# Kernel tuning notes

Hardware: AMD Instinct MI355X
Metric: run time of the kernel (lower is better)

## Reference

```python
import jax, jax.numpy as jnp
import numpy as np

DIM, HEADS, WS = 256, 16, 8
B, H, W = 2, 252, 252
BN_EPS = 1e-5


def _rel_index():
    # Same construction as the torch buffer relative_position_index (64,64)
    coords = np.stack(np.meshgrid(np.arange(WS), np.arange(WS), indexing='ij'))
    flat = coords.reshape(2, -1)
    rel = (flat[:, :, None] - flat[:, None, :]).transpose(1, 2, 0).copy()
    rel[..., 0] += WS - 1
    rel[..., 1] += WS - 1
    rel[..., 0] *= 2 * WS - 1
    return jnp.asarray(rel.sum(-1))

REL_IDX = _rel_index()  # (WS*WS, WS*WS) int


def _conv(x, w, pad, groups=1):
    return jax.lax.conv_general_dilated(
        x, w, (1, 1), [(pad[0], pad[0]), (pad[1], pad[1])],
        dimension_numbers=('NCHW', 'OIHW', 'NCHW'), feature_group_count=groups)


def setup_inputs() -> dict:
    key = jax.random.key(0)
    ks = jax.random.split(key, 8)
    s = lambda k, shape, sc: jax.random.normal(k, shape, jnp.float32) * sc
    z = lambda: jnp.zeros((DIM,), jnp.float32)
    return {
        'x': s(ks[0], (B, DIM, H, W), 1.0),
        'w_qkv': s(ks[1], (3 * DIM, DIM, 1, 1), 0.05),
        'rel_bias_table': s(ks[2], ((2 * WS - 1) ** 2, HEADS), 0.02),
        'w_h': s(ks[3], (DIM, DIM, WS, 1), 0.02),
        'b_h': z(),
        'w_v': s(ks[4], (DIM, DIM, 1, WS), 0.02),
        'b_v': z(),
        'w_dw': s(ks[5], (DIM, 1, WS, WS), 0.05),
        'bn_gamma': jnp.ones((DIM,), jnp.float32),
        'bn_beta': z(),
        'bn_mean': z(),
        'bn_var': jnp.ones((DIM,), jnp.float32),
        'w_pw': s(ks[6], (DIM, DIM, 1, 1), 0.05),
    }


def reference(x, w_qkv, rel_bias_table, w_h, b_h, w_v, b_v, w_dw,
              bn_gamma, bn_beta, bn_mean, bn_var, w_pw):
    Bc, C, Hc, Wc = x.shape
    pad_h, pad_w = WS - Hc % WS, WS - Wc % WS
    xp = jnp.pad(x, ((0, 0), (0, 0), (0, pad_h), (0, pad_w)), mode='reflect')
    Hp, Wp = Hc + pad_h, Wc + pad_w
    hh, ww, d = Hp // WS, Wp // WS, C // HEADS

    qkv = _conv(xp, w_qkv, (0, 0))  # (B, 3C, Hp, Wp)
    # b (qkv h d) (hh ws1) (ww ws2) -> qkv (b hh ww) h (ws1 ws2) d
    qkv = qkv.reshape(Bc, 3, HEADS, d, hh, WS, ww, WS)
    qkv = qkv.transpose(1, 0, 4, 6, 2, 5, 7, 3).reshape(3, Bc * hh * ww, HEADS, WS * WS, d)
    q, k, v = qkv[0], qkv[1], qkv[2]

    dots = jnp.einsum('nhid,nhjd->nhij', q, k) * (d ** -0.5)
    bias = rel_bias_table[REL_IDX.reshape(-1)].reshape(WS * WS, WS * WS, HEADS)
    dots = dots + bias.transpose(2, 0, 1)[None]  # (1, h, 64, 64)
    attn = jax.nn.softmax(dots, axis=-1)
    out = jnp.einsum('nhij,nhjd->nhid', attn, v)
    # (b hh ww) h (ws1 ws2) d -> b (h d) (hh ws1) (ww ws2)
    out = out.reshape(Bc, hh, ww, HEADS, WS, WS, d)
    out = out.transpose(0, 3, 6, 1, 4, 2, 5).reshape(Bc, C, Hp, Wp)
    out = out[:, :, :Hc, :Wc]

    p1 = _conv(jnp.pad(out, ((0, 0), (0, 0), (0, 1), (0, 0)), mode='reflect'),
               w_h, (WS // 2 - 1, 0)) + b_h[None, :, None, None]
    p2 = _conv(jnp.pad(out, ((0, 0), (0, 0), (0, 0), (0, 1)), mode='reflect'),
               w_v, (0, WS // 2 - 1)) + b_v[None, :, None, None]
    y = jnp.pad(p1 + p2, ((0, 0), (0, 0), (0, 1), (0, 1)), mode='reflect')
    y = _conv(y, w_dw, ((WS - 1) // 2, (WS - 1) // 2), groups=DIM)  # depthwise
    inv = bn_gamma / jnp.sqrt(bn_var + BN_EPS)
    y = y * inv[None, :, None, None] + (bn_beta - bn_mean * inv)[None, :, None, None]
    y = _conv(y, w_pw, (0, 0))  # pointwise 1x1
    return y[:, :, :Hc, :Wc]
```

## Files before the change

kernel.cpp:

```cpp
#include <hip/hip_runtime.h>
#include <hip/hip_bf16.h>

#define HC 252
#define WC 252
#define CD 256
#define NHEADS 16

#define XP_W 264
#define XP_HW (252*264)
#define XP_CHW (256*252*264)

typedef unsigned short u16;
typedef unsigned int u32;
typedef __attribute__((ext_vector_type(8))) short bf16x8;
typedef __attribute__((ext_vector_type(4))) float f32x4;
typedef __attribute__((ext_vector_type(4))) u32 u32x4;
typedef __attribute__((ext_vector_type(2))) u32 u32x2;

#define XP_BYTES (2u * (unsigned)XP_CHW * 2u)
#define ZP_OFF   XP_BYTES
#define ZP_BYTES 409600u
#define WT_OFF   (ZP_OFF + ZP_BYTES)
#define WT_ELEMS (128*8192)
#define WPW_OFF  (WT_OFF + (unsigned)WT_ELEMS*2u)
#define WPW_ELEMS (8*8192)
#define WQ_OFF   (WPW_OFF + (unsigned)WPW_ELEMS*2u)
#define WQ_ELEMS (768*256)
#define BIAS_OFF (WQ_OFF + (unsigned)WQ_ELEMS*2u)

__device__ __forceinline__ u16 bfu(float f) {
    __hip_bfloat16 h = __float2bfloat16(f);
    return *(reinterpret_cast<u16*>(&h));
}
__device__ __forceinline__ u32 pack2(float a, float b) {
    return (u32)bfu(a) | ((u32)bfu(b) << 16);
}

__global__ __launch_bounds__(256, 2) void attn_mfma(
    const float* __restrict__ x, const u16* __restrict__ WQ,
    const float* __restrict__ BIASF, u16* __restrict__ xp)
{
    __shared__ __align__(16) char smem[73728];

    const int bid = blockIdx.x;
    const int zz = (bid & 7) * 256 + (bid >> 3);
    const int wx = zz & 31, wy = (zz >> 5) & 31, b = zz >> 10;
    const int tid = threadIdx.x;
    const int lane = tid & 63, wid = tid >> 6;
    const int g = lane >> 4, li = lane & 15;

    {
        int ci = tid;
        const float* srcc = x + (size_t)(b * 256 + ci) * (HC * WC);
        #pragma unroll
        for (int r = 0; r < 8; ++r) {
            int h = wy * 8 + r; if (h >= HC) h = 2 * HC - 2 - h;
            const float* src = srcc + h * WC;
            float v[8];
            if (wx == 31) {
                #pragma unroll
                for (int c = 0; c < 8; ++c) {
                    int w = 248 + c; if (w >= WC) w = 2 * WC - 2 - w;
                    v[c] = src[w];
                }
            } else {
                float4 f0 = *(const float4*)(src + wx * 8);
                float4 f1 = *(const float4*)(src + wx * 8 + 4);
                v[0]=f0.x; v[1]=f0.y; v[2]=f0.z; v[3]=f0.w;
                v[4]=f1.x; v[5]=f1.y; v[6]=f1.z; v[7]=f1.w;
            }
            #pragma unroll
            for (int c = 0; c < 8; ++c) {
                int pos = r * 8 + c;
                int byte = pos * 512 + ((ci * 2) ^ ((pos & 7) << 4));
                *(u16*)(smem + byte) = bfu(v[c]);
            }
        }
    }
    __syncthreads();

    const int WB = 32768 + wid * 10240;
    char* Qb = smem + WB;
    char* Kb = smem + WB + 2048;
    char* Vb = smem + WB + 4096;
    char* Pb = smem + WB + 6144;

    const bf16x8 zf = {0,0,0,0,0,0,0,0};

    #pragma unroll 1
    for (int hh = 0; hh < 4; ++hh) {
        const int head = wid * 4 + hh;

        f32x4 acc[3][4];
        #pragma unroll
        for (int p = 0; p < 3; ++p)
            #pragma unroll
            for (int nf = 0; nf < 4; ++nf) acc[p][nf] = (f32x4){0.f,0.f,0.f,0.f};

        for (int ks = 0; ks < 8; ++ks) {
            bf16x8 bx[4];
            #pragma unroll
            for (int nf = 0; nf < 4; ++nf) {
                int pos = 16 * nf + li;
                int byte = pos * 512 + ((ks * 64 + 16 * g) ^ ((pos & 7) << 4));
                bx[nf] = *(const bf16x8*)(smem + byte);
            }
            bf16x8 aw[3];
            #pragma unroll
            for (int p = 0; p < 3; ++p) {
                int o = p * 256 + head * 16 + li;
                aw[p] = *(const bf16x8*)(WQ + o * 256 + ks * 32 + 8 * g);
            }
            __builtin_amdgcn_s_setprio(1);
            #pragma unroll
            for (int p = 0; p < 3; ++p)
                #pragma unroll
                for (int nf = 0; nf < 4; ++nf)
                    acc[p][nf] = __builtin_amdgcn_mfma_f32_16x16x32_bf16(aw[p], bx[nf], acc[p][nf], 0, 0, 0);
            __builtin_amdgcn_s_setprio(0);
        }

        #pragma unroll
        for (int p = 0; p < 3; ++p) {
            if (p < 2) {
                char* base = (p == 0) ? Qb : Kb;
                #pragma unroll
                for (int nf = 0; nf < 4; ++nf) {
                    int pos = 16 * nf + li;
                    u32 lo = pack2(acc[p][nf][0], acc[p][nf][1]);
                    u32 hi = pack2(acc[p][nf][2], acc[p][nf][3]);
                    int byte = pos * 32 + ((8 * g) ^ (((pos >> 2) & 1) << 4));
                    *(u32x2*)(base + byte) = (u32x2){lo, hi};
                }
            } else {
                #pragma unroll
                for (int nf = 0; nf < 4; ++nf) {
                    int pos = 16 * nf + li;
                    #pragma unroll
                    for (int r = 0; r < 4; ++r) {
                        int d = 4 * g + r;
                        int byte = (pos >> 3) * 256 + d * 16 + (pos & 7) * 2;
                        *(u16*)(Vb + byte) = bfu(acc[p][nf][r]);
                    }
                }
            }
        }

        f32x4 s[4][4];
        #pragma unroll
        for (int mf = 0; mf < 4; ++mf)
            #pragma unroll
            for (int nf = 0; nf < 4; ++nf) s[mf][nf] = (f32x4){0.f,0.f,0.f,0.f};
        bf16x8 bk[4];
        #pragma unroll
        for (int nf = 0; nf < 4; ++nf) {
            int pos = 16 * nf + li;
            bk[nf] = (g < 2) ? *(const bf16x8*)(Kb + pos * 32 + ((16 * g) ^ (((pos >> 2) & 1) << 4))) : zf;
        }
        __builtin_amdgcn_s_setprio(1);
        #pragma unroll
        for (int mf = 0; mf < 4; ++mf) {
            int pos = 16 * mf + li;
            bf16x8 aq = (g < 2) ? *(const bf16x8*)(Qb + pos * 32 + ((16 * g) ^ (((pos >> 2) & 1) << 4))) : zf;
            #pragma unroll
            for (int nf = 0; nf < 4; ++nf)
                s[mf][nf] = __builtin_amdgcn_mfma_f32_16x16x32_bf16(aq, bk[nf], s[mf][nf], 0, 0, 0);
        }
        __builtin_amdgcn_s_setprio(0);

        f32x4 e[4][4];
        f32x4 rs[4];
        #pragma unroll
        for (int mf = 0; mf < 4; ++mf) rs[mf] = (f32x4){0.f,0.f,0.f,0.f};
        #pragma unroll
        for (int mf = 0; mf < 4; ++mf)
            #pragma unroll
            for (int nf = 0; nf < 4; ++nf) {
                f32x4 b4 = *(const f32x4*)(BIASF + (((head * 4 + mf) * 4 + nf) * 64 + lane) * 4);
                #pragma unroll
                for (int r = 0; r < 4; ++r) {
                    float ev = __expf(s[mf][nf][r] * 0.25f + b4[r]);
                    e[mf][nf][r] = ev;
                    rs[mf][r] += ev;
                }
            }
        #pragma unroll
        for (int mf = 0; mf < 4; ++mf)
            #pragma unroll
            for (int r = 0; r < 4; ++r) {
                float t = rs[mf][r];
                t += __shfl_xor(t, 1); t += __shfl_xor(t, 2);
                t += __shfl_xor(t, 4); t += __shfl_xor(t, 8);
                rs[mf][r] = t;
            }

        f32x4 o[4];
        #pragma unroll
        for (int mf = 0; mf < 4; ++mf) o[mf] = (f32x4){0.f,0.f,0.f,0.f};
        const bool even = !(lane & 1);
        #pragma unroll
        for (int hf = 0; hf < 2; ++hf) {
            #pragma unroll
            for (int mf = 0; mf < 4; ++mf)
                #pragma unroll
                for (int nfl = 0; nfl < 2; ++nfl) {
                    f32x4 ee = e[mf][2 * hf + nfl];
                    float p0 = __shfl_xor(ee[0], 1), p1 = __shfl_xor(ee[1], 1);
                    float p2 = __shfl_xor(ee[2], 1), p3 = __shfl_xor(ee[3], 1);
                    int jl = 16 * nfl + (li & ~1);
                    u32 w0, w1; int r0;
                    if (even) { w0 = pack2(ee[0], p0); w1 = pack2(ee[1], p1); r0 = 0; }
                    else      { w0 = pack2(p2, ee[2]); w1 = pack2(p3, ee[3]); r0 = 2; }
                    int i0 = 16 * mf + 4 * g + r0, i1 = i0 + 1;
                    *(u32*)(Pb + i0 * 64 + ((2 * jl) ^ ((i0 & 3) << 4))) = w0;
                    *(u32*)(Pb + i1 * 64 + ((2 * jl) ^ ((i1 & 3) << 4))) = w1;
                }
            bf16x8 bv = *(const bf16x8*)(Vb + (4 * hf + g) * 256 + li * 16);
            __builtin_amdgcn_s_setprio(1);
            #pragma unroll
            for (int mf = 0; mf < 4; ++mf) {
                int i = 16 * mf + li;
                bf16x8 ap = *(const bf16x8*)(Pb + i * 64 + ((16 * g) ^ ((i & 3) << 4)));
                o[mf] = __builtin_amdgcn_mfma_f32_16x16x32_bf16(ap, bv, o[mf], 0, 0, 0);
            }
            __builtin_amdgcn_s_setprio(0);
        }

        #pragma unroll
        for (int mf = 0; mf < 4; ++mf) {
            int h = wy * 8 + 2 * mf + (g >> 1);
            int wbase = wx * 8 + 4 * (g & 1);
            if (h < HC && wbase < WC) {
                float v0 = o[mf][0] / rs[mf][0], v1 = o[mf][1] / rs[mf][1];
                float v2 = o[mf][2] / rs[mf][2], v3 = o[mf][3] / rs[mf][3];
                size_t idx = ((size_t)(b * 256 + head * 16 + li) * HC + h) * XP_W + wbase + 4;
                *(u32x2*)(xp + idx) = (u32x2){pack2(v0, v1), pack2(v2, v3)};
            }
        }
    }
}

__global__ __launch_bounds__(256) void wprep_kernel(
    const float* __restrict__ wh, const float* __restrict__ wv,
    const float* __restrict__ wpw, const float* __restrict__ wqkv,
    const float* __restrict__ btab, u16* __restrict__ wsu)
{
    int i = blockIdx.x * 256 + threadIdx.x;
    u16* WT = wsu + WT_OFF / 2;
    u16* WP = wsu + WPW_OFF / 2;
    u16* ZP = wsu + ZP_OFF / 2;
    u16* WQp = wsu + WQ_OFF / 2;
    float* BF = (float*)(wsu + BIAS_OFF / 2);
    if (i < WT_ELEMS) {
        int j = i & 7, co = (i >> 3) & 255, kb = (i >> 11) & 3, s = i >> 13;
        float v = (s < 64) ? wh[co * 2048 + s * 32 + kb * 8 + j]
                           : wv[co * 2048 + (s - 64) * 32 + kb * 8 + j];
        WT[i] = bfu(v);
    } else if (i < WT_ELEMS + WPW_ELEMS) {
        int i2 = i - WT_ELEMS;
        int j = i2 & 7, co = (i2 >> 3) & 255, kb = (i2 >> 11) & 3, s = i2 >> 13;
        WP[i2] = bfu(wpw[co * 256 + s * 32 + kb * 8 + j]);
    } else if (i < WT_ELEMS + WPW_ELEMS + (int)(ZP_BYTES / 2)) {
        ZP[i - WT_ELEMS - WPW_ELEMS] = 0;
    } else if (i < WT_ELEMS + WPW_ELEMS + (int)(ZP_BYTES / 2) + WQ_ELEMS) {
        int i4 = i - WT_ELEMS - WPW_ELEMS - (int)(ZP_BYTES / 2);
        WQp[i4] = bfu(wqkv[i4]);
    } else {
        int i5 = i - WT_ELEMS - WPW_ELEMS - (int)(ZP_BYTES / 2) - WQ_ELEMS;
        if (i5 < 16384) {
            int lane = i5 & 63, nf = (i5 >> 6) & 3, mf = (i5 >> 8) & 3, head = i5 >> 10;
            int gg = lane >> 4, ll = lane & 15;
            #pragma unroll
            for (int r = 0; r < 4; ++r) {
                int row = 16 * mf + 4 * gg + r;
                int col = 16 * nf + ll;
                int dy = (row >> 3) - (col >> 3) + 7;
                int dx = (row & 7) - (col & 7) + 7;
                BF[i5 * 4 + r] = btab[(dy * 15 + dx) * NHEADS + head];
            }
        }
    }
}

__global__ __launch_bounds__(256) void halo_kernel(u16* __restrict__ xp)
{
    int i = blockIdx.x * 256 + threadIdx.x;
    if (i >= 129024 * 12) return;
    int row = i / 12, c = i % 12;
    int wp = (c < 4) ? c : 252 + c;
    u16 v = 0;
    if (wp == 256) v = xp[row * XP_W + 254];
    xp[row * XP_W + wp] = v;
}

__global__ __launch_bounds__(512, 2) void sepconv_mfma(
    const u16* __restrict__ xp, const u16* __restrict__ WT,
    const u16* __restrict__ ZP,
    const float* __restrict__ b_h, const float* __restrict__ b_v,
    float* __restrict__ P)
{
    __shared__ u16 As[2][8192];
    __shared__ u16 Bs[2][256 * 36];

    const int bid = blockIdx.x;
    const int zz = (bid & 7) * 63 + (bid >> 3);
    const int h = zz % HC, b = zz / HC;
    const int tid = threadIdx.x;
    const int lane = tid & 63, wid = tid >> 6;
    const int wr = wid >> 2, wc = wid & 3;
    const int cq = lane & 15, kb = lane >> 4;

    const int wl2 = (tid & 127) * 2;
    const int oc = tid >> 7;

    const u16* hcur[8];
    int hstep[8];
    #pragma unroll
    for (int t = 0; t < 8; ++t) {
        int j = h + t - 3;
        bool valid = (j >= 0 && j <= 252);
        int jr = (j == 252) ? 250 : j;
        hcur[t] = valid ? (xp + (size_t)b * XP_CHW + (size_t)jr * XP_W) : ZP;
        hstep[t] = valid ? 4 * XP_HW : 0;
    }
    const u16* vbase = xp + (size_t)b * XP_CHW + (size_t)h * XP_W;
    const int hvoff = oc * XP_HW + wl2 + 4;

    const int bw0 = wl2 * 36 + oc * 8;
    const int bw1 = bw0 + 36;

    f32x4 acc[8][4];
    #pragma unroll
    for (int m = 0; m < 8; ++m)
        #pragma unroll
        for (int n = 0; n < 4; ++n) acc[m][n] = (f32x4){0.f, 0.f, 0.f, 0.f};

    u32x4 rA[2];
    u32 rB[8];

    int aw0, aw1;
    {
        int c0 = tid, c1 = 512 + tid;
        aw0 = ((c0 >> 8) * 256 + ((c0 & 255) ^ (((c0 >> 8) & 3) << 1))) * 8;
        aw1 = ((c1 >> 8) * 256 + ((c1 & 255) ^ (((c1 >> 8) & 3) << 1))) * 8;
    }

    rA[0] = *(const u32x4*)(WT + (size_t)tid * 8);
    rA[1] = *(const u32x4*)(WT + (size_t)(512 + tid) * 8);
    #pragma unroll
    for (int t = 0; t < 8; ++t)
        rB[t] = *(const u32*)(hcur[t] + hvoff);
    *(u32x4*)&As[0][aw0] = rA[0];
    *(u32x4*)&As[0][aw1] = rA[1];
    {
        union { bf16x8 v; u32 u[4]; } p0, p1;
        #pragma unroll
        for (int q = 0; q < 4; ++q) {
            p0.u[q] = __builtin_amdgcn_perm(rB[2 * q + 1], rB[2 * q], 0x05040100u);
            p1.u[q] = __builtin_amdgcn_perm(rB[2 * q + 1], rB[2 * q], 0x07060302u);
        }
        *(bf16x8*)&Bs[0][bw0] = p0.v;
        *(bf16x8*)&Bs[0][bw1] = p1.v;
    }

    for (int s = 0; s < 128; ++s) {
        const int cur = s & 1;
        const int s1 = s + 1;
        const bool hph1 = (s1 < 64);
        if (s1 < 128) {
            rA[0] = *(const u32x4*)(WT + (size_t)s1 * 8192 + (size_t)tid * 8);
            rA[1] = *(const u32x4*)(WT + (size_t)s1 * 8192 + (size_t)(512 + tid) * 8);
            if (hph1) {
                #pragma unroll
                for (int t = 0; t < 8; ++t) hcur[t] += hstep[t];
                #pragma unroll
                for (int t = 0; t < 8; ++t)
                    rB[t] = *(const u32*)(hcur[t] + hvoff);
            } else {
                int off = ((s1 - 64) * 4 + oc) * XP_HW + wl2;
                #pragma unroll
                for (int l = 0; l < 6; ++l)
                    rB[l] = *(const u32*)(vbase + off + 2 * l);
            }
        }
        __syncthreads();

        bf16x8 af[8], bfr[4];
        #pragma unroll
        for (int m = 0; m < 8; ++m) {
            int row = wr * 128 + m * 16 + cq;
            af[m] = *(const bf16x8*)&As[cur][(kb * 256 + (row ^ (kb << 1))) * 8];
        }
        #pragma unroll
        for (int n = 0; n < 4; ++n)
            bfr[n] = *(const bf16x8*)&Bs[cur][(wc * 64 + n * 16 + cq) * 36 + kb * 8];
        #pragma unroll
        for (int m = 0; m < 8; ++m)
            #pragma unroll
            for (int n = 0; n < 4; ++n)
                acc[m][n] = __builtin_amdgcn_mfma_f32_16x16x32_bf16(af[m], bfr[n], acc[m][n], 0, 0, 0);

        if (s1 < 128) {
            const int nxt = cur ^ 1;
            *(u32x4*)&As[nxt][aw0] = rA[0];
            *(u32x4*)&As[nxt][aw1] = rA[1];
            union { bf16x8 v; u32 u[4]; } p0, p1;
            if (hph1) {
                #pragma unroll
                for (int q = 0; q < 4; ++q) {
                    p0.u[q] = __builtin_amdgcn_perm(rB[2 * q + 1], rB[2 * q], 0x05040100u);
                    p1.u[q] = __builtin_amdgcn_perm(rB[2 * q + 1], rB[2 * q], 0x07060302u);
                }
            } else {
                #pragma unroll
                for (int q = 0; q < 4; ++q)
                    p0.u[q] = __builtin_amdgcn_alignbit(rB[q + 1], rB[q], 16);
                p1.u[0] = rB[1]; p1.u[1] = rB[2];
                p1.u[2] = rB[3]; p1.u[3] = rB[4];
            }
            *(bf16x8*)&Bs[nxt][bw0] = p0.v;
            *(bf16x8*)&Bs[nxt][bw1] = p1.v;
        }
    }

    const int rq = lane >> 4, cc = lane & 15;
    #pragma unroll
    for (int m = 0; m < 8; ++m) {
        int cgb = wr * 128 + m * 16 + rq * 4;
        float bias[4];
        #pragma unroll
        for (int rr = 0; rr < 4; ++rr) bias[rr] = b_h[cgb + rr] + b_v[cgb + rr];
        #pragma unroll
        for (int n = 0; n < 4; ++n) {
            int wg = wc * 64 + n * 16 + cc;
            if (wg < WC) {
                #pragma unroll
                for (int rr = 0; rr < 4; ++rr)
                    P[((size_t)(b * CD + cgb + rr) * HC + h) * WC + wg] = acc[m][n][rr] + bias[rr];
            }
        }
    }
}

__global__ __launch_bounds__(256) void dwbn_kernel(
    const float* __restrict__ P, const float* __restrict__ w_dw,
    const float* __restrict__ gamma, const float* __restrict__ beta,
    const float* __restrict__ mean, const float* __restrict__ var,
    __hip_bfloat16* __restrict__ Yb)
{
    __shared__ float ps[15][42];
    __shared__ float wd[64];
    const int bw = blockIdx.x, bh = blockIdx.y, bz = blockIdx.z;
    const int b = bz >> 8, c = bz & 255;
    const int h0 = bh * 8, w0 = bw * 32;
    const int tid = threadIdx.x;
    if (tid < 64) wd[tid] = w_dw[c * 64 + tid];
    for (int it = 0; it < 3; ++it) {
        int flat = tid + it * 256;
        if (flat < 630) {
            int row = flat / 42, col = flat % 42;
            int j = h0 - 3 + row, wcol = w0 - 3 + col;
            float v = 0.f;
            if (j >= 0 && j <= HC && wcol >= 0 && wcol <= WC) {
                int jr = (j == HC) ? (HC - 2) : j;
                int wr2 = (wcol == WC) ? (WC - 2) : wcol;
                v = P[((b * CD + c) * HC + jr) * WC + wr2];
            }
            ps[row][col] = v;
        }
    }
    __syncthreads();
    const int r = tid >> 5, cc = tid & 31;
    const int h = h0 + r, w = w0 + cc;
    if (h < HC && w < WC) {
        float s = 0.f;
        #pragma unroll
        for (int u = 0; u < 8; ++u)
            #pragma unroll
            for (int v2 = 0; v2 < 8; ++v2)
                s += wd[u * 8 + v2] * ps[r + u][cc + v2];
        const float inv = gamma[c] * rsqrtf(var[c] + 1e-5f);
        Yb[((b * CD + c) * HC + h) * WC + w] = __float2bfloat16(s * inv + (beta[c] - mean[c] * inv));
    }
}

__global__ __launch_bounds__(512, 2) void pw_mfma(
    const u16* __restrict__ Y, const u16* __restrict__ WP,
    float* __restrict__ O)
{
    __shared__ u16 As[2][8192];
    __shared__ u16 Bs[2][256 * 36];

    const int bid = blockIdx.x;
    const int zz = (bid & 7) * 63 + (bid >> 3);
    const int h = zz % HC, b = zz / HC;
    const int tid = threadIdx.x;
    const int lane = tid & 63, wid = tid >> 6;
    const int wr = wid >> 2, wc = wid & 3;
    const int cq = lane & 15, kb = lane >> 4;

    const int wl2 = (tid & 127) * 2;
    const int oc = tid >> 7;

    const u16* yb = Y + ((size_t)(b * 256 + oc * 8) * HC + h) * WC + wl2;

    const int bw0 = wl2 * 36 + oc * 8;
    const int bw1 = bw0 + 36;

    f32x4 acc[8][4];
    #pragma unroll
    for (int m = 0; m < 8; ++m)
        #pragma unroll
        for (int n = 0; n < 4; ++n) acc[m][n] = (f32x4){0.f, 0.f, 0.f, 0.f};

    u32x4 rA[2];
    u32 rB[8];

    int aw0, aw1;
    {
        int c0 = tid, c1 = 512 + tid;
        aw0 = ((c0 >> 8) * 256 + ((c0 & 255) ^ (((c0 >> 8) & 3) << 1))) * 8;
        aw1 = ((c1 >> 8) * 256 + ((c1 & 255) ^ (((c1 >> 8) & 3) << 1))) * 8;
    }

    rA[0] = *(const u32x4*)(WP + (size_t)tid * 8);
    rA[1] = *(const u32x4*)(WP + (size_t)(512 + tid) * 8);
    #pragma unroll
    for (int j = 0; j < 8; ++j)
        rB[j] = *(const u32*)(yb + (size_t)j * (HC * WC));
    *(u32x4*)&As[0][aw0] = rA[0];
    *(u32x4*)&As[0][aw1] = rA[1];
    {
        union { bf16x8 v; u32 u[4]; } p0, p1;
        #pragma unroll
        for (int q = 0; q < 4; ++q) {
            p0.u[q] = __builtin_amdgcn_perm(rB[2 * q + 1], rB[2 * q], 0x05040100u);
            p1.u[q] = __builtin_amdgcn_perm(rB[2 * q + 1], rB[2 * q], 0x07060302u);
        }
        *(bf16x8*)&Bs[0][bw0] = p0.v;
        *(bf16x8*)&Bs[0][bw1] = p1.v;
    }

    for (int s = 0; s < 8; ++s) {
        const int cur = s & 1;
        const int s1 = s + 1;
        if (s1 < 8) {
            rA[0] = *(const u32x4*)(WP + (size_t)s1 * 8192 + (size_t)tid * 8);
            rA[1] = *(const u32x4*)(WP + (size_t)s1 * 8192 + (size_t)(512 + tid) * 8);
            #pragma unroll
            for (int j = 0; j < 8; ++j)
                rB[j] = *(const u32*)(yb + (size_t)(s1 * 32 + j) * (HC * WC));
        }
        __syncthreads();

        bf16x8 af[8], bfr[4];
        #pragma unroll
        for (int m = 0; m < 8; ++m) {
            int row = wr * 128 + m * 16 + cq;
            af[m] = *(const bf16x8*)&As[cur][(kb * 256 + (row ^ (kb << 1))) * 8];
        }
        #pragma unroll
        for (int n = 0; n < 4; ++n)
            bfr[n] = *(const bf16x8*)&Bs[cur][(wc * 64 + n * 16 + cq) * 36 + kb * 8];
        #pragma unroll
        for (int m = 0; m < 8; ++m)
            #pragma unroll
            for (int n = 0; n < 4; ++n)
                acc[m][n] = __builtin_amdgcn_mfma_f32_16x16x32_bf16(af[m], bfr[n], acc[m][n], 0, 0, 0);

        if (s1 < 8) {
            const int nxt = cur ^ 1;
            *(u32x4*)&As[nxt][aw0] = rA[0];
            *(u32x4*)&As[nxt][aw1] = rA[1];
            union { bf16x8 v; u32 u[4]; } p0, p1;
            #pragma unroll
            for (int q = 0; q < 4; ++q) {
                p0.u[q] = __builtin_amdgcn_perm(rB[2 * q + 1], rB[2 * q], 0x05040100u);
                p1.u[q] = __builtin_amdgcn_perm(rB[2 * q + 1], rB[2 * q], 0x07060302u);
            }
            *(bf16x8*)&Bs[nxt][bw0] = p0.v;
            *(bf16x8*)&Bs[nxt][bw1] = p1.v;
        }
    }

    const int rq = lane >> 4, cc = lane & 15;
    #pragma unroll
    for (int m = 0; m < 8; ++m) {
        int cgb = wr * 128 + m * 16 + rq * 4;
        #pragma unroll
        for (int n = 0; n < 4; ++n) {
            int wg = wc * 64 + n * 16 + cc;
            if (wg < WC) {
                #pragma unroll
                for (int rr = 0; rr < 4; ++rr)
                    O[((size_t)(b * CD + cgb + rr) * HC + h) * WC + wg] = acc[m][n][rr];
            }
        }
    }
}

extern "C" void kernel_launch(void* const* d_in, const int* in_sizes, int n_in,
                              void* d_out, int out_size, void* d_ws, size_t ws_size,
                              hipStream_t stream)
{
    const float* x      = (const float*)d_in[0];
    const float* w_qkv  = (const float*)d_in[1];
    const float* bias_t = (const float*)d_in[2];
    const float* w_h    = (const float*)d_in[3];
    const float* b_h    = (const float*)d_in[4];
    const float* w_v    = (const float*)d_in[5];
    const float* b_v    = (const float*)d_in[6];
    const float* w_dw   = (const float*)d_in[7];
    const float* bn_g   = (const float*)d_in[8];
    const float* bn_b   = (const float*)d_in[9];
    const float* bn_m   = (const float*)d_in[10];
    const float* bn_v   = (const float*)d_in[11];
    const float* w_pw   = (const float*)d_in[12];
    float* out = (float*)d_out;

    u16* wsu = (u16*)d_ws;
    const u16* XPu = wsu;
    const u16* ZPu = wsu + ZP_OFF / 2;
    const u16* WTu = wsu + WT_OFF / 2;
    const u16* WPu = wsu + WPW_OFF / 2;
    const u16* WQu = wsu + WQ_OFF / 2;
    const float* BFu = (const float*)(wsu + BIAS_OFF / 2);

    wprep_kernel<<<5984, 256, 0, stream>>>(w_h, w_v, w_pw, w_qkv, bias_t, wsu);
    attn_mfma<<<2048, 256, 0, stream>>>(x, WQu, BFu, wsu);
    halo_kernel<<<6048, 256, 0, stream>>>(wsu);
    sepconv_mfma<<<504, 512, 0, stream>>>(XPu, WTu, ZPu, b_h, b_v, out);
    dwbn_kernel<<<dim3(8, 32, 512), 256, 0, stream>>>(out, w_dw, bn_g, bn_b, bn_m, bn_v,
                                                      (__hip_bfloat16*)d_ws);
    pw_mfma<<<504, 512, 0, stream>>>(wsu, WPu, out);
}
```

Measured before the change: 677.1 us.

## Store sepconv output as bf16, pre-swizzle weights, raise MFMA priority

The separable-conv intermediate P is now written as bf16 instead of fp32 and converted back in the depthwise/BN kernel, halving that round-trip's memory traffic at a small precision cost. Weight tiles for sepconv and pointwise GEMMs are pre-swizzled in the prep kernel, so the LDS stores use a linear address and the per-thread swizzle math goes away. The MFMA blocks are wrapped in s_setprio raises, and the main loops are marked unroll 1 to limit code size and register pressure.

```diff
diff --git a/kernel.cpp b/kernel.cpp
--- a/kernel.cpp
+++ b/kernel.cpp
@@ -34,6 +34,9 @@
 }
 __device__ __forceinline__ u32 pack2(float a, float b) {
     return (u32)bfu(a) | ((u32)bfu(b) << 16);
+}
+__device__ __forceinline__ float bf2f(u16 v) {
+    union { u32 u; float f; } cv; cv.u = ((u32)v) << 16; return cv.f;
 }
 
 __global__ __launch_bounds__(256, 2) void attn_mfma(
@@ -252,13 +255,17 @@
     u16* WQp = wsu + WQ_OFF / 2;
     float* BF = (float*)(wsu + BIAS_OFF / 2);
     if (i < WT_ELEMS) {
-        int j = i & 7, co = (i >> 3) & 255, kb = (i >> 11) & 3, s = i >> 13;
+        int j = i & 7, l = (i >> 3) & 1023, s = i >> 13;
+        int kb = (l >> 8) & 3;
+        int co = (l & 255) ^ (kb << 1);
         float v = (s < 64) ? wh[co * 2048 + s * 32 + kb * 8 + j]
                            : wv[co * 2048 + (s - 64) * 32 + kb * 8 + j];
         WT[i] = bfu(v);
     } else if (i < WT_ELEMS + WPW_ELEMS) {
         int i2 = i - WT_ELEMS;
-        int j = i2 & 7, co = (i2 >> 3) & 255, kb = (i2 >> 11) & 3, s = i2 >> 13;
+        int j = i2 & 7, l = (i2 >> 3) & 1023, s = i2 >> 13;
+        int kb = (l >> 8) & 3;
+        int co = (l & 255) ^ (kb << 1);
         WP[i2] = bfu(wpw[co * 256 + s * 32 + kb * 8 + j]);
     } else if (i < WT_ELEMS + WPW_ELEMS + (int)(ZP_BYTES / 2)) {
         ZP[i - WT_ELEMS - WPW_ELEMS] = 0;
@@ -297,10 +304,10 @@
     const u16* __restrict__ xp, const u16* __restrict__ WT,
     const u16* __restrict__ ZP,
     const float* __restrict__ b_h, const float* __restrict__ b_v,
-    float* __restrict__ P)
+    u16* __restrict__ P)
 {
-    __shared__ u16 As[2][8192];
-    __shared__ u16 Bs[2][256 * 36];
+    __shared__ __align__(16) u16 As[2][8192];
+    __shared__ __align__(16) u16 Bs[2][256 * 36];
 
     const int bid = blockIdx.x;
     const int zz = (bid & 7) * 63 + (bid >> 3);
@@ -338,20 +345,13 @@
     u32x4 rA[2];
     u32 rB[8];
 
-    int aw0, aw1;
-    {
-        int c0 = tid, c1 = 512 + tid;
-        aw0 = ((c0 >> 8) * 256 + ((c0 & 255) ^ (((c0 >> 8) & 3) << 1))) * 8;
-        aw1 = ((c1 >> 8) * 256 + ((c1 & 255) ^ (((c1 >> 8) & 3) << 1))) * 8;
-    }
-
     rA[0] = *(const u32x4*)(WT + (size_t)tid * 8);
     rA[1] = *(const u32x4*)(WT + (size_t)(512 + tid) * 8);
     #pragma unroll
     for (int t = 0; t < 8; ++t)
         rB[t] = *(const u32*)(hcur[t] + hvoff);
-    *(u32x4*)&As[0][aw0] = rA[0];
-    *(u32x4*)&As[0][aw1] = rA[1];
+    *(u32x4*)&As[0][(size_t)tid * 8] = rA[0];
+    *(u32x4*)&As[0][(size_t)(512 + tid) * 8] = rA[1];
     {
         union { bf16x8 v; u32 u[4]; } p0, p1;
         #pragma unroll
@@ -363,6 +363,7 @@
         *(bf16x8*)&Bs[0][bw1] = p1.v;
     }
 
+    #pragma unroll 1
     for (int s = 0; s < 128; ++s) {
         const int cur = s & 1;
         const int s1 = s + 1;
@@ -385,25 +386,29 @@
         }
         __syncthreads();
 
-        bf16x8 af[8], bfr[4];
-        #pragma unroll
-        for (int m = 0; m < 8; ++m) {
-            int row = wr * 128 + m * 16 + cq;
-            af[m] = *(const bf16x8*)&As[cur][(kb * 256 + (row ^ (kb << 1))) * 8];
-        }
-        #pragma unroll
-        for (int n = 0; n < 4; ++n)
-            bfr[n] = *(const bf16x8*)&Bs[cur][(wc * 64 + n * 16 + cq) * 36 + kb * 8];
-        #pragma unroll
-        for (int m = 0; m < 8; ++m)
+        {
+            bf16x8 af[8], bfr[4];
+            #pragma unroll
+            for (int m = 0; m < 8; ++m) {
+                int row = wr * 128 + m * 16 + cq;
+                af[m] = *(const bf16x8*)&As[cur][(kb * 256 + (row ^ (kb << 1))) * 8];
+            }
             #pragma unroll
             for (int n = 0; n < 4; ++n)
-                acc[m][n] = __builtin_amdgcn_mfma_f32_16x16x32_bf16(af[m], bfr[n], acc[m][n], 0, 0, 0);
+                bfr[n] = *(const bf16x8*)&Bs[cur][(wc * 64 + n * 16 + cq) * 36 + kb * 8];
+            __builtin_amdgcn_s_setprio(1);
+            #pragma unroll
+            for (int m = 0; m < 8; ++m)
+                #pragma unroll
+                for (int n = 0; n < 4; ++n)
+                    acc[m][n] = __builtin_amdgcn_mfma_f32_16x16x32_bf16(af[m], bfr[n], acc[m][n], 0, 0, 0);
+            __builtin_amdgcn_s_setprio(0);
+        }
 
         if (s1 < 128) {
             const int nxt = cur ^ 1;
-            *(u32x4*)&As[nxt][aw0] = rA[0];
-            *(u32x4*)&As[nxt][aw1] = rA[1];
+            *(u32x4*)&As[nxt][(size_t)tid * 8] = rA[0];
+            *(u32x4*)&As[nxt][(size_t)(512 + tid) * 8] = rA[1];
             union { bf16x8 v; u32 u[4]; } p0, p1;
             if (hph1) {
                 #pragma unroll
@@ -436,14 +441,14 @@
             if (wg < WC) {
                 #pragma unroll
                 for (int rr = 0; rr < 4; ++rr)
-                    P[((size_t)(b * CD + cgb + rr) * HC + h) * WC + wg] = acc[m][n][rr] + bias[rr];
+                    P[((size_t)(b * CD + cgb + rr) * HC + h) * WC + wg] = bfu(acc[m][n][rr] + bias[rr]);
             }
         }
     }
 }
 
 __global__ __launch_bounds__(256) void dwbn_kernel(
-    const float* __restrict__ P, const float* __restrict__ w_dw,
+    const u16* __restrict__ P, const float* __restrict__ w_dw,
     const float* __restrict__ gamma, const float* __restrict__ beta,
     const float* __restrict__ mean, const float* __restrict__ var,
     __hip_bfloat16* __restrict__ Yb)
@@ -464,7 +469,7 @@
             if (j >= 0 && j <= HC && wcol >= 0 && wcol <= WC) {
                 int jr = (j == HC) ? (HC - 2) : j;
                 int wr2 = (wcol == WC) ? (WC - 2) : wcol;
-                v = P[((b * CD + c) * HC + jr) * WC + wr2];
+                v = bf2f(P[((size_t)(b * CD + c) * HC + jr) * WC + wr2]);
             }
             ps[row][col] = v;
         }
@@ -488,8 +493,8 @@
     const u16* __restrict__ Y, const u16* __restrict__ WP,
     float* __restrict__ O)
 {
-    __shared__ u16 As[2][8192];
-    __shared__ u16 Bs[2][256 * 36];
+    __shared__ __align__(16) u16 As[2][8192];
+    __shared__ __align__(16) u16 Bs[2][256 * 36];
 
     const int bid = blockIdx.x;
     const int zz = (bid & 7) * 63 + (bid >> 3);
@@ -516,20 +521,13 @@
     u32x4 rA[2];
     u32 rB[8];
 
-    int aw0, aw1;
-    {
-        int c0 = tid, c1 = 512 + tid;
-        aw0 = ((c0 >> 8) * 256 + ((c0 & 255) ^ (((c0 >> 8) & 3) << 1))) * 8;
-        aw1 = ((c1 >> 8) * 256 + ((c1 & 255) ^ (((c1 >> 8) & 3) << 1))) * 8;
-    }
-
     rA[0] = *(const u32x4*)(WP + (size_t)tid * 8);
     rA[1] = *(const u32x4*)(WP + (size_t)(512 + tid) * 8);
     #pragma unroll
     for (int j = 0; j < 8; ++j)
         rB[j] = *(const u32*)(yb + (size_t)j * (HC * WC));
-    *(u32x4*)&As[0][aw0] = rA[0];
-    *(u32x4*)&As[0][aw1] = rA[1];
+    *(u32x4*)&As[0][(size_t)tid * 8] = rA[0];
+    *(u32x4*)&As[0][(size_t)(512 + tid) * 8] = rA[1];
     {
         union { bf16x8 v; u32 u[4]; } p0, p1;
         #pragma unroll
@@ -541,6 +539,7 @@
         *(bf16x8*)&Bs[0][bw1] = p1.v;
     }
 
+    #pragma unroll 1
     for (int s = 0; s < 8; ++s) {
         const int cur = s & 1;
         const int s1 = s + 1;
@@ -553,25 +552,29 @@
         }
         __syncthreads();
 
-        bf16x8 af[8], bfr[4];
-        #pragma unroll
-        for (int m = 0; m < 8; ++m) {
-            int row = wr * 128 + m * 16 + cq;
-            af[m] = *(const bf16x8*)&As[cur][(kb * 256 + (row ^ (kb << 1))) * 8];
-        }
-        #pragma unroll
-        for (int n = 0; n < 4; ++n)
-            bfr[n] = *(const bf16x8*)&Bs[cur][(wc * 64 + n * 16 + cq) * 36 + kb * 8];
-        #pragma unroll
-        for (int m = 0; m < 8; ++m)
+        {
+            bf16x8 af[8], bfr[4];
+            #pragma unroll
+            for (int m = 0; m < 8; ++m) {
+                int row = wr * 128 + m * 16 + cq;
+                af[m] = *(const bf16x8*)&As[cur][(kb * 256 + (row ^ (kb << 1))) * 8];
+            }
             #pragma unroll
             for (int n = 0; n < 4; ++n)
-                acc[m][n] = __builtin_amdgcn_mfma_f32_16x16x32_bf16(af[m], bfr[n], acc[m][n], 0, 0, 0);
+                bfr[n] = *(const bf16x8*)&Bs[cur][(wc * 64 + n * 16 + cq) * 36 + kb * 8];
+            __builtin_amdgcn_s_setprio(1);
+            #pragma unroll
+            for (int m = 0; m < 8; ++m)
+                #pragma unroll
+                for (int n = 0; n < 4; ++n)
+                    acc[m][n] = __builtin_amdgcn_mfma_f32_16x16x32_bf16(af[m], bfr[n], acc[m][n], 0, 0, 0);
+            __builtin_amdgcn_s_setprio(0);
+        }
 
         if (s1 < 8) {
             const int nxt = cur ^ 1;
-            *(u32x4*)&As[nxt][aw0] = rA[0];
-            *(u32x4*)&As[nxt][aw1] = rA[1];
+            *(u32x4*)&As[nxt][(size_t)tid * 8] = rA[0];
+            *(u32x4*)&As[nxt][(size_t)(512 + tid) * 8] = rA[1];
             union { bf16x8 v; u32 u[4]; } p0, p1;
             #pragma unroll
             for (int q = 0; q < 4; ++q) {
@@ -629,8 +632,8 @@
     wprep_kernel<<<5984, 256, 0, stream>>>(w_h, w_v, w_pw, w_qkv, bias_t, wsu);
     attn_mfma<<<2048, 256, 0, stream>>>(x, WQu, BFu, wsu);
     halo_kernel<<<6048, 256, 0, stream>>>(wsu);
-    sepconv_mfma<<<504, 512, 0, stream>>>(XPu, WTu, ZPu, b_h, b_v, out);
-    dwbn_kernel<<<dim3(8, 32, 512), 256, 0, stream>>>(out, w_dw, bn_g, bn_b, bn_m, bn_v,
-                                                      (__hip_bfloat16*)d_ws);
+    sepconv_mfma<<<504, 512, 0, stream>>>(XPu, WTu, ZPu, b_h, b_v, (u16*)d_out);
+    dwbn_kernel<<<dim3(8, 32, 512), 256, 0, stream>>>((const u16*)d_out, w_dw, bn_g, bn_b,
+                                                      bn_m, bn_v, (__hip_bfloat16*)d_ws);
     pw_mfma<<<504, 512, 0, stream>>>(wsu, WPu, out);
 }
```

Result: no change. 678.1 us (+0.1%).
